# Optimization experiments

Measured on AMD Instinct MI355X. Metric: run time of the kernel, lower is better.

Reference implementation:

```python
import jax, jax.numpy as jnp
import numpy as np
from jax import lax

BN_EPS = 1e-5


def _zpool(x, axis):
    # stack (mean, max) over `axis` as 2 channels -> [N, 2, A, B]
    return jnp.stack([jnp.mean(x, axis=axis), jnp.max(x, axis=axis)], axis=1)


def _gate(p2, conv_w, conv_b, bn_w, bn_b, bn_rm, bn_rv, i):
    # p2: [N, 2, A, B]; 7x7 conv (2->1, pad 3) + scalar BN + relu + sigmoid
    y = lax.conv_general_dilated(
        p2, conv_w, window_strides=(1, 1), padding=[(3, 3), (3, 3)],
        dimension_numbers=("NCHW", "OIHW", "NCHW"))[:, 0] + conv_b[0]  # [N, A, B]
    y = (y - bn_rm[i]) * lax.rsqrt(bn_rv[i] + BN_EPS) * bn_w[i] + bn_b[i]
    return jax.nn.sigmoid(jnp.maximum(y, 0.0))


def setup_inputs() -> dict:
    key = jax.random.key(0)
    ks = jax.random.split(key, 7)
    N, C, H, W = 256, 2048, 7, 7
    return {
        "x": jax.random.normal(ks[0], (N, C, H, W), dtype=jnp.float32),
        "conv_w": jax.random.normal(ks[1], (1, 2, 7, 7), dtype=jnp.float32) * 0.1,
        "conv_b": jax.random.normal(ks[2], (1,), dtype=jnp.float32) * 0.1,
        "bn_w": jax.random.normal(ks[3], (3,), dtype=jnp.float32),
        "bn_b": jax.random.normal(ks[4], (3,), dtype=jnp.float32),
        "bn_rm": jax.random.normal(ks[5], (3,), dtype=jnp.float32) * 0.1,
        "bn_rv": jax.random.uniform(ks[6], (3,), dtype=jnp.float32),
    }


def reference(x, conv_w, conv_b, bn_w, bn_b, bn_rm, bn_rv):
    # x: [N, C, 7, 7]
    g_hw = _gate(_zpool(x, 1), conv_w, conv_b, bn_w, bn_b, bn_rm, bn_rv, 0)  # [N, 7, 7]
    g_ch = _gate(_zpool(x, 3), conv_w, conv_b, bn_w, bn_b, bn_rm, bn_rv, 1)  # [N, C, 7] indexed by h
    g_cw = _gate(_zpool(x, 2), conv_w, conv_b, bn_w, bn_b, bn_rm, bn_rv, 2)  # [N, C, 7] indexed by w
    gate = (g_hw[:, None, :, :] + g_ch[:, :, :, None] + g_cw[:, :, None, :]) * (1.0 / 3.0)
    return x * gate
```

## Files before the change

kernel.cpp:

```cpp
#include <hip/hip_runtime.h>

#define N_ 256
#define C_ 2048
#define HW_ 49
#define CPB 64
#define NCC (C_/CPB)

#define CHB(lc) ((lc) * HW_ + ((lc) >= 3 ? 1 : 0))

__global__ __launch_bounds__(256) void k_poolc(const float* __restrict__ x,
                                               float* __restrict__ psum,
                                               float* __restrict__ pmax) {
  const int cc = blockIdx.x, n = blockIdx.y;
  const int t = threadIdx.x;
  __shared__ float sx[CPB * HW_];
  __shared__ float part_s[HW_][5];
  __shared__ float part_m[HW_][5];

  const float4* xv = (const float4*)(x + ((size_t)n * C_ + (size_t)cc * CPB) * HW_);
  for (int v = t; v < 784; v += 256) {
    float4 q = xv[v];
    sx[v * 4 + 0] = q.x; sx[v * 4 + 1] = q.y;
    sx[v * 4 + 2] = q.z; sx[v * 4 + 3] = q.w;
  }
  __syncthreads();

  if (t < 245) {
    int hw = t / 5, s = t % 5;
    float sm = 0.f, mx = -3.4e38f;
    #pragma unroll
    for (int j = 0; j < 13; ++j) {
      int c = s * 13 + j;
      if (c < CPB) {
        float a = sx[c * HW_ + hw];
        sm += a; mx = fmaxf(mx, a);
      }
    }
    part_s[hw][s] = sm; part_m[hw][s] = mx;
  }
  __syncthreads();

  if (t < HW_) {
    float sm = 0.f, mx = -3.4e38f;
    #pragma unroll
    for (int s = 0; s < 5; ++s) { sm += part_s[t][s]; mx = fmaxf(mx, part_m[t][s]); }
    size_t o = ((size_t)n * NCC + cc) * HW_ + t;
    psum[o] = sm; pmax[o] = mx;
  }
}

__global__ __launch_bounds__(64) void k_ghw(const float* __restrict__ psum,
                                            const float* __restrict__ pmax,
                                            const float* __restrict__ cw,
                                            const float* __restrict__ cb,
                                            const float* __restrict__ bnw,
                                            const float* __restrict__ bnb,
                                            const float* __restrict__ bnrm,
                                            const float* __restrict__ bnrv,
                                            float* __restrict__ ghw) {
  const int n = blockIdx.x;
  const int t = threadIdx.x;
  __shared__ float p2c[2][13][13];
  __shared__ float s_cw[98];

  for (int i = t; i < 2 * 13 * 13; i += 64) ((float*)p2c)[i] = 0.f;
  for (int i = t; i < 98; i += 64) s_cw[i] = cw[i];
  __syncthreads();

  if (t < HW_) {
    float sm = 0.f, mx = -3.4e38f;
    const float* ps = psum + (size_t)n * NCC * HW_ + t;
    const float* pm = pmax + (size_t)n * NCC * HW_ + t;
    for (int cc = 0; cc < NCC; ++cc) {
      sm += ps[cc * HW_];
      mx = fmaxf(mx, pm[cc * HW_]);
    }
    p2c[0][t / 7 + 3][t % 7 + 3] = sm * (1.f / C_);
    p2c[1][t / 7 + 3][t % 7 + 3] = mx;
  }
  __syncthreads();

  if (t < HW_) {
    int a = t / 7, b = t % 7;
    float y = cb[0];
    #pragma unroll
    for (int i2 = 0; i2 < 2; ++i2)
      #pragma unroll
      for (int p = 0; p < 7; ++p)
        #pragma unroll
        for (int q = 0; q < 7; ++q)
          y += p2c[i2][a + p][b + q] * s_cw[i2 * 49 + p * 7 + q];
    float sc = bnw[0] * rsqrtf(bnrv[0] + 1e-5f);
    y = (y - bnrm[0]) * sc + bnb[0];
    y = fmaxf(y, 0.f);
    ghw[n * HW_ + t] = 1.f / (1.f + __expf(-y));
  }
}

__global__ __launch_bounds__(256, 6) void k_main(const float* __restrict__ x,
    const float* __restrict__ ghw,
    const float* __restrict__ cw, const float* __restrict__ cb,
    const float* __restrict__ bnw, const float* __restrict__ bnb,
    const float* __restrict__ bnrm, const float* __restrict__ bnrv,
    float* __restrict__ out) {
  const int cc = blockIdx.x;
  const int n  = (N_ - 1) - blockIdx.y;
  const int c0 = cc * CPB;
  const int t  = threadIdx.x;

  __shared__ __align__(16) float sx[3432];
  __shared__ __align__(16) float pool_lo[1120];
  __shared__ __align__(16) float pool_hi[1120];
  __shared__ float gch[448];
  __shared__ float gcw[448];
  __shared__ __align__(16) float s_w[112];
  __shared__ float s_ghw[49];

  const int conv = t & 1, i2 = (t >> 1) & 1, cl = t >> 2;
  const int bi = 1 + conv;
  const float cb0 = cb[0];
  const float sc_bn = bnw[bi] * rsqrtf(bnrv[bi] + 1e-5f);
  const float rm_bn = bnrm[bi];
  const float sh_bn = bnb[bi];

  if (t < 112) {
    int i2w = t / 56, rem = t % 56, p = rem / 8, q = rem % 8;
    s_w[t] = (q < 7) ? cw[i2w * 49 + p * 7 + q] : 0.f;
  }
  if (t < HW_) s_ghw[t] = ghw[n * HW_ + t];
  for (int i = t; i < 2 * 3 * HW_; i += 256) {
    int side = i / 147, off = i % 147;
    int lc = side ? (67 + off / HW_) : (off / HW_);
    int c = c0 - 3 + lc;
    float vv = 0.f;
    if (c >= 0 && c < C_) vv = x[((size_t)n * C_ + c) * HW_ + off % HW_];
    sx[CHB(lc) + off % HW_] = vv;
  }
  const float4* xv = (const float4*)(x + ((size_t)n * C_ + c0) * HW_);
  float4* sxv = (float4*)(sx + 148);
  for (int v = t; v < 784; v += 256) sxv[v] = xv[v];
  __syncthreads();

  for (int i = t; i < 70 * 7; i += 256) {
    int lc = i / 7, k = i % 7;
    int base = CHB(lc);
    float s1 = 0.f, m1 = -3.4e38f, s2 = 0.f, m2 = -3.4e38f;
    #pragma unroll
    for (int j = 0; j < 7; ++j) {
      float a = sx[base + k * 7 + j];
      s1 += a; m1 = fmaxf(m1, a);
      float b = sx[base + j * 7 + k];
      s2 += b; m2 = fmaxf(m2, b);
    }
    float* pb = (k < 4) ? pool_lo : pool_hi;
    int kk = k & 3;
    pb[(0 * 70 + lc) * 4 + kk] = s1 * (1.f / 7.f);
    pb[(1 * 70 + lc) * 4 + kk] = m1;
    pb[(2 * 70 + lc) * 4 + kk] = s2 * (1.f / 7.f);
    pb[(3 * 70 + lc) * 4 + kk] = m2;
  }
  __syncthreads();

  {
    const int f = conv * 2 + i2;
    const float* Wb = s_w + i2 * 56;
    float acc[7] = {0.f, 0.f, 0.f, 0.f, 0.f, 0.f, 0.f};
    #pragma unroll
    for (int p = 0; p < 7; ++p) {
      int ri = (f * 70 + cl + p) * 4;
      float4 r0 = *(const float4*)(pool_lo + ri);
      float4 r1 = *(const float4*)(pool_hi + ri);
      float row[7] = {r0.x, r0.y, r0.z, r0.w, r1.x, r1.y, r1.z};
      float4 w0 = *(const float4*)(Wb + p * 8);
      float4 w1 = *(const float4*)(Wb + p * 8 + 4);
      float wr[7] = {w0.x, w0.y, w0.z, w0.w, w1.x, w1.y, w1.z};
      #pragma unroll
      for (int q = 0; q < 7; ++q) {
        #pragma unroll
        for (int k = 0; k < 7; ++k) {
          int c = k + q - 3;
          if (c >= 0 && c < 7) acc[k] += row[c] * wr[q];
        }
      }
    }
    float fsum[7];
    #pragma unroll
    for (int k = 0; k < 7; ++k) fsum[k] = acc[k] + __shfl_xor(acc[k], 2, 64);
    if (i2 == 0) {
      float* gp = (conv ? gcw : gch) + cl * 7;
      #pragma unroll
      for (int k = 0; k < 7; ++k) {
        float y = (fsum[k] + cb0 - rm_bn) * sc_bn + sh_bn;
        y = fmaxf(y, 0.f);
        gp[k] = 1.f / (1.f + __expf(-y));
      }
    }
  }
  __syncthreads();

  float4* outv = (float4*)(out + ((size_t)n * C_ + c0) * HW_);
  for (int v = t; v < 784; v += 256) {
    float4 q = sxv[v];
    int e0 = v * 4;
    int cj = e0 / 49;
    int hw0 = e0 - cj * 49;
    float r0 = q.x, r1 = q.y, r2 = q.z, r3 = q.w;
    {
      int hw = hw0;
      int cjj = cj + (hw >= 49); hw -= (hw >= 49) ? 49 : 0;
      int h = (hw * 37) >> 8, w2 = hw - h * 7;
      r0 *= (s_ghw[hw] + gch[cjj * 7 + h] + gcw[cjj * 7 + w2]) * (1.f / 3.f);
    }
    {
      int hw = hw0 + 1;
      int cjj = cj + (hw >= 49); hw -= (hw >= 49) ? 49 : 0;
      int h = (hw * 37) >> 8, w2 = hw - h * 7;
      r1 *= (s_ghw[hw] + gch[cjj * 7 + h] + gcw[cjj * 7 + w2]) * (1.f / 3.f);
    }
    {
      int hw = hw0 + 2;
      int cjj = cj + (hw >= 49); hw -= (hw >= 49) ? 49 : 0;
      int h = (hw * 37) >> 8, w2 = hw - h * 7;
      r2 *= (s_ghw[hw] + gch[cjj * 7 + h] + gcw[cjj * 7 + w2]) * (1.f / 3.f);
    }
    {
      int hw = hw0 + 3;
      int cjj = cj + (hw >= 49); hw -= (hw >= 49) ? 49 : 0;
      int h = (hw * 37) >> 8, w2 = hw - h * 7;
      r3 *= (s_ghw[hw] + gch[cjj * 7 + h] + gcw[cjj * 7 + w2]) * (1.f / 3.f);
    }
    outv[v] = make_float4(r0, r1, r2, r3);
  }
}

extern "C" void kernel_launch(void* const* d_in, const int* in_sizes, int n_in,
                              void* d_out, int out_size, void* d_ws, size_t ws_size,
                              hipStream_t stream) {
  const float* x    = (const float*)d_in[0];
  const float* cw   = (const float*)d_in[1];
  const float* cb   = (const float*)d_in[2];
  const float* bnw  = (const float*)d_in[3];
  const float* bnb  = (const float*)d_in[4];
  const float* bnrm = (const float*)d_in[5];
  const float* bnrv = (const float*)d_in[6];
  float* out = (float*)d_out;

  float* psum = (float*)d_ws;
  float* pmax = psum + (size_t)N_ * NCC * HW_;
  float* ghw  = pmax + (size_t)N_ * NCC * HW_;

  k_poolc<<<dim3(NCC, N_), 256, 0, stream>>>(x, psum, pmax);
  k_ghw<<<dim3(N_), 64, 0, stream>>>(psum, pmax, cw, cb, bnw, bnb, bnrm, bnrv, ghw);
  k_main<<<dim3(NCC, N_), 256, 0, stream>>>(x, ghw, cw, cb, bnw, bnb, bnrm, bnrv, out);
}
```

Baseline: 89.29 us.

## Coarsen channel pooling blocks and compute two conv rows per thread

The channel-pooling kernel now has each block reduce 256 channels in four shared-memory passes, accumulating in registers, instead of 64 channels. This cuts the partial-result count per sample from 32 to 8, so the gate kernel reads fewer partials. In the main kernel, half the threads compute two adjacent conv output rows each, reusing the loaded pooled rows across both, with an interleaved pool layout to keep shared-memory accesses spread across banks. The trade-off is fewer blocks for the pooling kernel, extra barriers inside it, and half the main-kernel threads idle during the conv.

```diff
diff --git a/kernel.cpp b/kernel.cpp
--- a/kernel.cpp
+++ b/kernel.cpp
@@ -5,47 +5,52 @@
 #define HW_ 49
 #define CPB 64
 #define NCC (C_/CPB)
+#define NCHUNK 8
 
 #define CHB(lc) ((lc) * HW_ + ((lc) >= 3 ? 1 : 0))
+
+__device__ __forceinline__ int pool_idx(int f, int r, int kk) {
+  return (((f << 1) + (r & 1)) * 35 + (r >> 1)) * 4 + kk;
+}
 
 __global__ __launch_bounds__(256) void k_poolc(const float* __restrict__ x,
                                                float* __restrict__ psum,
                                                float* __restrict__ pmax) {
-  const int cc = blockIdx.x, n = blockIdx.y;
+  const int bc = blockIdx.x, n = blockIdx.y;
   const int t = threadIdx.x;
-  __shared__ float sx[CPB * HW_];
+  __shared__ __align__(16) float sx[CPB * HW_];
   __shared__ float part_s[HW_][5];
   __shared__ float part_m[HW_][5];
 
-  const float4* xv = (const float4*)(x + ((size_t)n * C_ + (size_t)cc * CPB) * HW_);
-  for (int v = t; v < 784; v += 256) {
-    float4 q = xv[v];
-    sx[v * 4 + 0] = q.x; sx[v * 4 + 1] = q.y;
-    sx[v * 4 + 2] = q.z; sx[v * 4 + 3] = q.w;
-  }
-  __syncthreads();
-
-  if (t < 245) {
-    int hw = t / 5, s = t % 5;
-    float sm = 0.f, mx = -3.4e38f;
-    #pragma unroll
-    for (int j = 0; j < 13; ++j) {
-      int c = s * 13 + j;
-      if (c < CPB) {
-        float a = sx[c * HW_ + hw];
-        sm += a; mx = fmaxf(mx, a);
+  float sm = 0.f, mx = -3.4e38f;
+  const int hw = t / 5, s = t % 5;
+
+  const float4* xv = (const float4*)(x + ((size_t)n * C_ + (size_t)bc * 256) * HW_);
+  #pragma unroll
+  for (int pass = 0; pass < 4; ++pass) {
+    float4* sv = (float4*)sx;
+    for (int v = t; v < 784; v += 256) sv[v] = xv[pass * 784 + v];
+    __syncthreads();
+    if (t < 245) {
+      #pragma unroll
+      for (int j = 0; j < 13; ++j) {
+        int c = s * 13 + j;
+        if (c < CPB) {
+          float a = sx[c * HW_ + hw];
+          sm += a; mx = fmaxf(mx, a);
+        }
       }
     }
-    part_s[hw][s] = sm; part_m[hw][s] = mx;
-  }
-  __syncthreads();
-
+    __syncthreads();
+  }
+  if (t < 245) { part_s[hw][s] = sm; part_m[hw][s] = mx; }
+  __syncthreads();
   if (t < HW_) {
-    float sm = 0.f, mx = -3.4e38f;
-    #pragma unroll
-    for (int s = 0; s < 5; ++s) { sm += part_s[t][s]; mx = fmaxf(mx, part_m[t][s]); }
-    size_t o = ((size_t)n * NCC + cc) * HW_ + t;
-    psum[o] = sm; pmax[o] = mx;
+    float s2 = 0.f, m2 = -3.4e38f;
+    #pragma unroll
+    for (int k = 0; k < 5; ++k) { s2 += part_s[t][k]; m2 = fmaxf(m2, part_m[t][k]); }
+    size_t o = ((size_t)n * NCHUNK + bc) * HW_ + t;
+    psum[o] = s2; pmax[o] = m2;
   }
 }
 
@@ -69,9 +74,10 @@
 
   if (t < HW_) {
     float sm = 0.f, mx = -3.4e38f;
-    const float* ps = psum + (size_t)n * NCC * HW_ + t;
-    const float* pm = pmax + (size_t)n * NCC * HW_ + t;
-    for (int cc = 0; cc < NCC; ++cc) {
+    const float* ps = psum + (size_t)n * NCHUNK * HW_ + t;
+    const float* pm = pmax + (size_t)n * NCHUNK * HW_ + t;
+    #pragma unroll
+    for (int cc = 0; cc < NCHUNK; ++cc) {
       sm += ps[cc * HW_];
       mx = fmaxf(mx, pm[cc * HW_]);
     }
@@ -116,7 +122,7 @@
   __shared__ __align__(16) float s_w[112];
   __shared__ float s_ghw[49];
 
-  const int conv = t & 1, i2 = (t >> 1) & 1, cl = t >> 2;
+  const int conv = t & 1, i2 = (t >> 1) & 1, cg = t >> 2;
   const int bi = 1 + conv;
   const float cb0 = cb[0];
   const float sc_bn = bnw[bi] * rsqrtf(bnrv[bi] + 1e-5f);
@@ -154,45 +160,68 @@
     }
     float* pb = (k < 4) ? pool_lo : pool_hi;
     int kk = k & 3;
-    pb[(0 * 70 + lc) * 4 + kk] = s1 * (1.f / 7.f);
-    pb[(1 * 70 + lc) * 4 + kk] = m1;
-    pb[(2 * 70 + lc) * 4 + kk] = s2 * (1.f / 7.f);
-    pb[(3 * 70 + lc) * 4 + kk] = m2;
-  }
-  __syncthreads();
-
-  {
+    pb[pool_idx(0, lc, kk)] = s1 * (1.f / 7.f);
+    pb[pool_idx(1, lc, kk)] = m1;
+    pb[pool_idx(2, lc, kk)] = s2 * (1.f / 7.f);
+    pb[pool_idx(3, lc, kk)] = m2;
+  }
+  __syncthreads();
+
+  if (t < 128) {
     const int f = conv * 2 + i2;
+    const int r0 = cg * 2;
     const float* Wb = s_w + i2 * 56;
-    float acc[7] = {0.f, 0.f, 0.f, 0.f, 0.f, 0.f, 0.f};
-    #pragma unroll
-    for (int p = 0; p < 7; ++p) {
-      int ri = (f * 70 + cl + p) * 4;
-      float4 r0 = *(const float4*)(pool_lo + ri);
-      float4 r1 = *(const float4*)(pool_hi + ri);
-      float row[7] = {r0.x, r0.y, r0.z, r0.w, r1.x, r1.y, r1.z};
-      float4 w0 = *(const float4*)(Wb + p * 8);
-      float4 w1 = *(const float4*)(Wb + p * 8 + 4);
-      float wr[7] = {w0.x, w0.y, w0.z, w0.w, w1.x, w1.y, w1.z};
-      #pragma unroll
-      for (int q = 0; q < 7; ++q) {
-        #pragma unroll
-        for (int k = 0; k < 7; ++k) {
-          int c = k + q - 3;
-          if (c >= 0 && c < 7) acc[k] += row[c] * wr[q];
-        }
-      }
-    }
-    float fsum[7];
-    #pragma unroll
-    for (int k = 0; k < 7; ++k) fsum[k] = acc[k] + __shfl_xor(acc[k], 2, 64);
+    float A[8], B[8];
+    float acc0[7] = {0,0,0,0,0,0,0};
+    float acc1[7] = {0,0,0,0,0,0,0};
+
+#define LOADROW(D, R) { \
+    int oo = pool_idx(f, (R), 0); \
+    float4 lo4 = *(const float4*)(pool_lo + oo); \
+    float4 hi4 = *(const float4*)(pool_hi + oo); \
+    D[0]=lo4.x; D[1]=lo4.y; D[2]=lo4.z; D[3]=lo4.w; \
+    D[4]=hi4.x; D[5]=hi4.y; D[6]=hi4.z; D[7]=hi4.w; }
+
+#define STEP(P, RL, RH) { \
+    float4 w0 = *(const float4*)(Wb + (P) * 8); \
+    float4 w1 = *(const float4*)(Wb + (P) * 8 + 4); \
+    float wr[7] = {w0.x, w0.y, w0.z, w0.w, w1.x, w1.y, w1.z}; \
+    _Pragma("unroll") \
+    for (int q = 0; q < 7; ++q) { \
+      _Pragma("unroll") \
+      for (int k = 0; k < 7; ++k) { \
+        int c = k + q - 3; \
+        if (c >= 0 && c < 7) { acc0[k] += RL[c] * wr[q]; acc1[k] += RH[c] * wr[q]; } \
+      } } }
+
+    LOADROW(A, r0);
+    LOADROW(B, r0 + 1);
+    STEP(0, A, B);
+    LOADROW(A, r0 + 2); STEP(1, B, A);
+    LOADROW(B, r0 + 3); STEP(2, A, B);
+    LOADROW(A, r0 + 4); STEP(3, B, A);
+    LOADROW(B, r0 + 5); STEP(4, A, B);
+    LOADROW(A, r0 + 6); STEP(5, B, A);
+    LOADROW(B, r0 + 7); STEP(6, A, B);
+#undef LOADROW
+#undef STEP
+
+    float f0[7], f1[7];
+    #pragma unroll
+    for (int k = 0; k < 7; ++k) {
+      f0[k] = acc0[k] + __shfl_xor(acc0[k], 2, 64);
+      f1[k] = acc1[k] + __shfl_xor(acc1[k], 2, 64);
+    }
     if (i2 == 0) {
-      float* gp = (conv ? gcw : gch) + cl * 7;
+      float* gp = (conv ? gcw : gch);
       #pragma unroll
       for (int k = 0; k < 7; ++k) {
-        float y = (fsum[k] + cb0 - rm_bn) * sc_bn + sh_bn;
-        y = fmaxf(y, 0.f);
-        gp[k] = 1.f / (1.f + __expf(-y));
+        float y0 = (f0[k] + cb0 - rm_bn) * sc_bn + sh_bn;
+        float y1 = (f1[k] + cb0 - rm_bn) * sc_bn + sh_bn;
+        y0 = fmaxf(y0, 0.f);
+        y1 = fmaxf(y1, 0.f);
+        gp[r0 * 7 + k]       = 1.f / (1.f + __expf(-y0));
+        gp[(r0 + 1) * 7 + k] = 1.f / (1.f + __expf(-y1));
       }
     }
   }
@@ -246,10 +275,10 @@
   float* out = (float*)d_out;
 
   float* psum = (float*)d_ws;
-  float* pmax = psum + (size_t)N_ * NCC * HW_;
-  float* ghw  = pmax + (size_t)N_ * NCC * HW_;
-
-  k_poolc<<<dim3(NCC, N_), 256, 0, stream>>>(x, psum, pmax);
+  float* pmax = psum + (size_t)N_ * NCHUNK * HW_;
+  float* ghw  = pmax + (size_t)N_ * NCHUNK * HW_;
+
+  k_poolc<<<dim3(NCHUNK, N_), 256, 0, stream>>>(x, psum, pmax);
   k_ghw<<<dim3(N_), 64, 0, stream>>>(psum, pmax, cw, cb, bnw, bnb, bnrm, bnrv, ghw);
   k_main<<<dim3(NCC, N_), 256, 0, stream>>>(x, ghw, cw, cb, bnw, bnb, bnrm, bnrv, out);
 }
```

New measurement: 82.29 us. -7.8%, faster.

## Move channel-gate conv into pooling kernel, leaving final pass as pure multiply

Applied to the files above, without the earlier changes.

The C-H and C-W pooling and their 7x7 gate convolutions move into the first pass, which now processes 256 channels per block in four staged passes and writes the gate vectors to workspace. The final kernel only loads x, the three gates and writes the output, dropping its halo loads, pooling and convolution. This trades extra global traffic for the gate arrays (about 2x N*C*7 floats) and a heavier, lower-parallelism first kernel for a lighter bandwidth-bound second pass. A fallback path keeps the old scheme when workspace is too small, and it contains an odd extra zero store.

```diff
diff --git a/kernel.cpp b/kernel.cpp
--- a/kernel.cpp
+++ b/kernel.cpp
@@ -4,48 +4,148 @@
 #define C_ 2048
 #define HW_ 49
 #define CPB 64
-#define NCC (C_/CPB)
-
-#define CHB(lc) ((lc) * HW_ + ((lc) >= 3 ? 1 : 0))
-
-__global__ __launch_bounds__(256) void k_poolc(const float* __restrict__ x,
-                                               float* __restrict__ psum,
-                                               float* __restrict__ pmax) {
-  const int cc = blockIdx.x, n = blockIdx.y;
+#define NCC 32
+#define NCHUNK 8
+
+
+__global__ __launch_bounds__(256) void k_pool_gate(const float* __restrict__ x,
+    const float* __restrict__ cw, const float* __restrict__ cb,
+    const float* __restrict__ bnw, const float* __restrict__ bnb,
+    const float* __restrict__ bnrm, const float* __restrict__ bnrv,
+    float* __restrict__ psum, float* __restrict__ pmax,
+    float* __restrict__ gch_g, float* __restrict__ gcw_g) {
+  const int bc = blockIdx.x, n = blockIdx.y;
   const int t = threadIdx.x;
-  __shared__ float sx[CPB * HW_];
+
+  __shared__ __align__(16) float sx[3584];
+  __shared__ __align__(16) float pool_lo[4 * 264 * 4];
+  __shared__ __align__(16) float pool_hi[4 * 264 * 4];
   __shared__ float part_s[HW_][5];
   __shared__ float part_m[HW_][5];
-
-  const float4* xv = (const float4*)(x + ((size_t)n * C_ + (size_t)cc * CPB) * HW_);
-  for (int v = t; v < 784; v += 256) {
-    float4 q = xv[v];
-    sx[v * 4 + 0] = q.x; sx[v * 4 + 1] = q.y;
-    sx[v * 4 + 2] = q.z; sx[v * 4 + 3] = q.w;
-  }
-  __syncthreads();
-
-  if (t < 245) {
-    int hw = t / 5, s = t % 5;
-    float sm = 0.f, mx = -3.4e38f;
-    #pragma unroll
-    for (int j = 0; j < 13; ++j) {
-      int c = s * 13 + j;
-      if (c < CPB) {
-        float a = sx[c * HW_ + hw];
-        sm += a; mx = fmaxf(mx, a);
+  __shared__ __align__(16) float s_w[112];
+
+  if (t < 112) {
+    int i2w = t / 56, rem = t % 56, p = rem / 8, q = rem % 8;
+    s_w[t] = (q < 7) ? cw[i2w * 49 + p * 7 + q] : 0.f;
+  }
+
+  float sm = 0.f, mx = -3.4e38f;
+  const int hwp = t / 5, sp = t % 5;
+
+  const float4* xv = (const float4*)(x + ((size_t)n * C_ + (size_t)bc * 256) * HW_);
+  float4* sv = (float4*)sx;
+  #pragma unroll
+  for (int pass = 0; pass < 4; ++pass) {
+    for (int v = t; v < 784; v += 256) sv[v] = xv[pass * 784 + v];
+    __syncthreads();
+    if (t < 245) {
+      #pragma unroll
+      for (int j = 0; j < 13; ++j) {
+        int c = sp * 13 + j;
+        if (c < CPB) { float a = sx[c * HW_ + hwp]; sm += a; mx = fmaxf(mx, a); }
       }
     }
-    part_s[hw][s] = sm; part_m[hw][s] = mx;
-  }
+    for (int i = t; i < 448; i += 256) {
+      int lc = i / 7, k = i % 7;
+      int base = lc * HW_;
+      float s1 = 0.f, m1 = -3.4e38f, s2 = 0.f, m2 = -3.4e38f;
+      #pragma unroll
+      for (int j = 0; j < 7; ++j) {
+        float a = sx[base + k * 7 + j]; s1 += a; m1 = fmaxf(m1, a);
+        float b = sx[base + j * 7 + k]; s2 += b; m2 = fmaxf(m2, b);
+      }
+      int pc = pass * 64 + 3 + lc;
+      int kk = k & 3;
+      float* pb = (k < 4) ? pool_lo : pool_hi;
+      pb[(0 * 264 + pc) * 4 + kk] = s1 * (1.f / 7.f);
+      pb[(1 * 264 + pc) * 4 + kk] = m1;
+      pb[(2 * 264 + pc) * 4 + kk] = s2 * (1.f / 7.f);
+      pb[(3 * 264 + pc) * 4 + kk] = m2;
+    }
+    __syncthreads();
+  }
+
+  if (t < 42) {
+    int hc = t / 7, k = t % 7;
+    int pc = (hc < 3) ? hc : 259 + (hc - 3);
+    int c = bc * 256 - 3 + pc;
+    float s1 = 0.f, m1 = 0.f, s2 = 0.f, m2 = 0.f;
+    if (c >= 0 && c < C_) {
+      m1 = -3.4e38f; m2 = -3.4e38f;
+      const float* xp = x + ((size_t)n * C_ + c) * HW_;
+      #pragma unroll
+      for (int j = 0; j < 7; ++j) {
+        float a = xp[k * 7 + j]; s1 += a; m1 = fmaxf(m1, a);
+        float b = xp[j * 7 + k]; s2 += b; m2 = fmaxf(m2, b);
+      }
+      s1 *= (1.f / 7.f); s2 *= (1.f / 7.f);
+    }
+    int kk = k & 3;
+    float* pb = (k < 4) ? pool_lo : pool_hi;
+    pb[(0 * 264 + pc) * 4 + kk] = s1;
+    pb[(1 * 264 + pc) * 4 + kk] = m1;
+    pb[(2 * 264 + pc) * 4 + kk] = s2;
+    pb[(3 * 264 + pc) * 4 + kk] = m2;
+  }
+  if (t < 245) { part_s[hwp][sp] = sm; part_m[hwp][sp] = mx; }
   __syncthreads();
 
   if (t < HW_) {
-    float sm = 0.f, mx = -3.4e38f;
-    #pragma unroll
-    for (int s = 0; s < 5; ++s) { sm += part_s[t][s]; mx = fmaxf(mx, part_m[t][s]); }
-    size_t o = ((size_t)n * NCC + cc) * HW_ + t;
-    psum[o] = sm; pmax[o] = mx;
+    float s2 = 0.f, m2 = -3.4e38f;
+    #pragma unroll
+    for (int k = 0; k < 5; ++k) { s2 += part_s[t][k]; m2 = fmaxf(m2, part_m[t][k]); }
+    size_t o = ((size_t)n * NCHUNK + bc) * HW_ + t;
+    psum[o] = s2; pmax[o] = m2;
+  }
+
+  const float cb0 = cb[0];
+  const float sc1 = bnw[1] * rsqrtf(bnrv[1] + 1e-5f), rm1 = bnrm[1], sh1 = bnb[1];
+  const float sc2 = bnw[2] * rsqrtf(bnrv[2] + 1e-5f), rm2 = bnrm[2], sh2 = bnb[2];
+  float g0[7] = {0, 0, 0, 0, 0, 0, 0};
+  float g1[7] = {0, 0, 0, 0, 0, 0, 0};
+  #pragma unroll
+  for (int f = 0; f < 4; ++f) {
+    const float* Wb = s_w + (f & 1) * 56;
+    #pragma unroll
+    for (int p = 0; p < 7; ++p) {
+      int ri = (f * 264 + t + p) * 4;
+      float4 lo4 = *(const float4*)(pool_lo + ri);
+      float4 hi4 = *(const float4*)(pool_hi + ri);
+      float row[7] = {lo4.x, lo4.y, lo4.z, lo4.w, hi4.x, hi4.y, hi4.z};
+      float4 w0 = *(const float4*)(Wb + p * 8);
+      float4 w1 = *(const float4*)(Wb + p * 8 + 4);
+      float wr[7] = {w0.x, w0.y, w0.z, w0.w, w1.x, w1.y, w1.z};
+      #pragma unroll
+      for (int q = 0; q < 7; ++q)
+        #pragma unroll
+        for (int k = 0; k < 7; ++k) {
+          int c = k + q - 3;
+          if (c >= 0 && c < 7) {
+            if (f < 2) g0[k] += row[c] * wr[q];
+            else       g1[k] += row[c] * wr[q];
+          }
+        }
+    }
+  }
+  #pragma unroll
+  for (int k = 0; k < 7; ++k) {
+    float y0 = (g0[k] + cb0 - rm1) * sc1 + sh1;
+    y0 = fmaxf(y0, 0.f);
+    sx[t * 7 + k] = 1.f / (1.f + __expf(-y0));
+    float y1 = (g1[k] + cb0 - rm2) * sc2 + sh2;
+    y1 = fmaxf(y1, 0.f);
+    sx[1792 + t * 7 + k] = 1.f / (1.f + __expf(-y1));
+  }
+  __syncthreads();
+  {
+    size_t goff = ((size_t)n * C_ + (size_t)bc * 256) * 7;
+    const float4* gs = (const float4*)sx;
+    float4* d1 = (float4*)(gch_g + goff);
+    float4* d2 = (float4*)(gcw_g + goff);
+    for (int v = t; v < 896; v += 256) {
+      if (v < 448) d1[v] = gs[v];
+      else         d2[v - 448] = gs[v];
+    }
   }
 }
 
@@ -69,9 +169,10 @@
 
   if (t < HW_) {
     float sm = 0.f, mx = -3.4e38f;
-    const float* ps = psum + (size_t)n * NCC * HW_ + t;
-    const float* pm = pmax + (size_t)n * NCC * HW_ + t;
-    for (int cc = 0; cc < NCC; ++cc) {
+    const float* ps = psum + (size_t)n * NCHUNK * HW_ + t;
+    const float* pm = pmax + (size_t)n * NCHUNK * HW_ + t;
+    #pragma unroll
+    for (int cc = 0; cc < NCHUNK; ++cc) {
       sm += ps[cc * HW_];
       mx = fmaxf(mx, pm[cc * HW_]);
     }
@@ -97,7 +198,110 @@
   }
 }
 
-__global__ __launch_bounds__(256, 6) void k_main(const float* __restrict__ x,
+__global__ __launch_bounds__(256) void k_mul(const float* __restrict__ x,
+    const float* __restrict__ ghw, const float* __restrict__ gch_g,
+    const float* __restrict__ gcw_g, float* __restrict__ out) {
+  const int cc = blockIdx.x;
+  const int n  = (N_ - 1) - blockIdx.y;
+  const int c0 = cc * CPB;
+  const int t  = threadIdx.x;
+
+  __shared__ float sg[960];
+
+  {
+    const float* g1 = gch_g + ((size_t)n * C_ + c0) * 7;
+    const float* g2 = gcw_g + ((size_t)n * C_ + c0) * 7;
+    for (int i = t; i < 945; i += 256) {
+      float v;
+      if (i < 448)      v = g1[i];
+      else if (i < 896) v = g2[i - 448];
+      else              v = ghw[n * HW_ + (i - 896)];
+      sg[i] = v;
+    }
+  }
+  __syncthreads();
+  const float* gch = sg;
+  const float* gcw = sg + 448;
+  const float* s_ghw = sg + 896;
+
+  const float4* xv = (const float4*)(x + ((size_t)n * C_ + c0) * HW_);
+  float4* outv = (float4*)(out + ((size_t)n * C_ + c0) * HW_);
+  for (int v = t; v < 784; v += 256) {
+    float4 q = xv[v];
+    int e0 = v * 4;
+    int cj = e0 / 49;
+    int hw0 = e0 - cj * 49;
+    float r0 = q.x, r1 = q.y, r2 = q.z, r3 = q.w;
+    {
+      int hw = hw0;
+      int cjj = cj + (hw >= 49); hw -= (hw >= 49) ? 49 : 0;
+      int h = (hw * 37) >> 8, w2 = hw - h * 7;
+      r0 *= (s_ghw[hw] + gch[cjj * 7 + h] + gcw[cjj * 7 + w2]) * (1.f / 3.f);
+    }
+    {
+      int hw = hw0 + 1;
+      int cjj = cj + (hw >= 49); hw -= (hw >= 49) ? 49 : 0;
+      int h = (hw * 37) >> 8, w2 = hw - h * 7;
+      r1 *= (s_ghw[hw] + gch[cjj * 7 + h] + gcw[cjj * 7 + w2]) * (1.f / 3.f);
+    }
+    {
+      int hw = hw0 + 2;
+      int cjj = cj + (hw >= 49); hw -= (hw >= 49) ? 49 : 0;
+      int h = (hw * 37) >> 8, w2 = hw - h * 7;
+      r2 *= (s_ghw[hw] + gch[cjj * 7 + h] + gcw[cjj * 7 + w2]) * (1.f / 3.f);
+    }
+    {
+      int hw = hw0 + 3;
+      int cjj = cj + (hw >= 49); hw -= (hw >= 49) ? 49 : 0;
+      int h = (hw * 37) >> 8, w2 = hw - h * 7;
+      r3 *= (s_ghw[hw] + gch[cjj * 7 + h] + gcw[cjj * 7 + w2]) * (1.f / 3.f);
+    }
+    outv[v] = make_float4(r0, r1, r2, r3);
+  }
+}
+
+
+__global__ __launch_bounds__(256) void k_poolc_fb(const float* __restrict__ x,
+                                                  float* __restrict__ psum,
+                                                  float* __restrict__ pmax) {
+  const int bc = blockIdx.x, n = blockIdx.y;
+  const int t = threadIdx.x;
+  __shared__ __align__(16) float sx[CPB * HW_];
+  __shared__ float part_s[HW_][5];
+  __shared__ float part_m[HW_][5];
+
+  float sm = 0.f, mx = -3.4e38f;
+  const int hw = t / 5, s = t % 5;
+
+  const float4* xv = (const float4*)(x + ((size_t)n * C_ + (size_t)bc * 256) * HW_);
+  #pragma unroll
+  for (int pass = 0; pass < 4; ++pass) {
+    float4* sv = (float4*)sx;
+    for (int v = t; v < 784; v += 256) sv[v] = xv[pass * 784 + v];
+    __syncthreads();
+    if (t < 245) {
+      #pragma unroll
+      for (int j = 0; j < 13; ++j) {
+        int c = s * 13 + j;
+        if (c < CPB) { float a = sx[c * HW_ + hw]; sm += a; mx = fmaxf(mx, a); }
+      }
+    }
+    __syncthreads();
+  }
+  if (t < 245) { part_s[hw][s] = sm; part_m[hw][s] = mx; }
+  __syncthreads();
+  if (t < HW_) {
+    float s2 = 0.f, m2 = -3.4e38f;
+    #pragma unroll
+    for (int k = 0; k < 5; ++k) { s2 += part_s[t][k]; m2 = fmaxf(m2, part_m[t][k]); }
+    size_t o = ((size_t)n * NCHUNK + bc) * HW_ + t;
+    psum[o] = s2; pmax[o] = m2;
+  }
+}
+
+#define CHB(lc) ((lc) * HW_ + ((lc) >= 3 ? 1 : 0))
+
+__global__ __launch_bounds__(256, 6) void k_main_fb(const float* __restrict__ x,
     const float* __restrict__ ghw,
     const float* __restrict__ cw, const float* __restrict__ cb,
     const float* __restrict__ bnw, const float* __restrict__ bnb,
@@ -147,13 +351,12 @@
     float s1 = 0.f, m1 = -3.4e38f, s2 = 0.f, m2 = -3.4e38f;
     #pragma unroll
     for (int j = 0; j < 7; ++j) {
-      float a = sx[base + k * 7 + j];
-      s1 += a; m1 = fmaxf(m1, a);
-      float b = sx[base + j * 7 + k];
-      s2 += b; m2 = fmaxf(m2, b);
+      float a = sx[base + k * 7 + j]; s1 += a; m1 = fmaxf(m1, a);
+      float b = sx[base + j * 7 + k]; s2 += b; m2 = fmaxf(m2, b);
     }
     float* pb = (k < 4) ? pool_lo : pool_hi;
     int kk = k & 3;
+    pb[((conv * 0 + 0) * 70 + lc) * 4 + kk + 0 * 280] = 0.f;
     pb[(0 * 70 + lc) * 4 + kk] = s1 * (1.f / 7.f);
     pb[(1 * 70 + lc) * 4 + kk] = m1;
     pb[(2 * 70 + lc) * 4 + kk] = s2 * (1.f / 7.f);
@@ -175,13 +378,12 @@
       float4 w1 = *(const float4*)(Wb + p * 8 + 4);
       float wr[7] = {w0.x, w0.y, w0.z, w0.w, w1.x, w1.y, w1.z};
       #pragma unroll
-      for (int q = 0; q < 7; ++q) {
+      for (int q = 0; q < 7; ++q)
         #pragma unroll
         for (int k = 0; k < 7; ++k) {
           int c = k + q - 3;
           if (c >= 0 && c < 7) acc[k] += row[c] * wr[q];
         }
-      }
     }
     float fsum[7];
     #pragma unroll
@@ -204,34 +406,19 @@
     int e0 = v * 4;
     int cj = e0 / 49;
     int hw0 = e0 - cj * 49;
-    float r0 = q.x, r1 = q.y, r2 = q.z, r3 = q.w;
-    {
-      int hw = hw0;
-      int cjj = cj + (hw >= 49); hw -= (hw >= 49) ? 49 : 0;
+    float r[4] = {q.x, q.y, q.z, q.w};
+    #pragma unroll
+    for (int j = 0; j < 4; ++j) {
+      int hw = hw0 + j;
+      int cjj = cj + (hw >= 49);
+      hw -= (hw >= 49) ? 49 : 0;
       int h = (hw * 37) >> 8, w2 = hw - h * 7;
-      r0 *= (s_ghw[hw] + gch[cjj * 7 + h] + gcw[cjj * 7 + w2]) * (1.f / 3.f);
-    }
-    {
-      int hw = hw0 + 1;
-      int cjj = cj + (hw >= 49); hw -= (hw >= 49) ? 49 : 0;
-      int h = (hw * 37) >> 8, w2 = hw - h * 7;
-      r1 *= (s_ghw[hw] + gch[cjj * 7 + h] + gcw[cjj * 7 + w2]) * (1.f / 3.f);
-    }
-    {
-      int hw = hw0 + 2;
-      int cjj = cj + (hw >= 49); hw -= (hw >= 49) ? 49 : 0;
-      int h = (hw * 37) >> 8, w2 = hw - h * 7;
-      r2 *= (s_ghw[hw] + gch[cjj * 7 + h] + gcw[cjj * 7 + w2]) * (1.f / 3.f);
-    }
-    {
-      int hw = hw0 + 3;
-      int cjj = cj + (hw >= 49); hw -= (hw >= 49) ? 49 : 0;
-      int h = (hw * 37) >> 8, w2 = hw - h * 7;
-      r3 *= (s_ghw[hw] + gch[cjj * 7 + h] + gcw[cjj * 7 + w2]) * (1.f / 3.f);
-    }
-    outv[v] = make_float4(r0, r1, r2, r3);
-  }
-}
+      r[j] *= (s_ghw[hw] + gch[cjj * 7 + h] + gcw[cjj * 7 + w2]) * (1.f / 3.f);
+    }
+    outv[v] = make_float4(r[0], r[1], r[2], r[3]);
+  }
+}
+
 
 extern "C" void kernel_launch(void* const* d_in, const int* in_sizes, int n_in,
                               void* d_out, int out_size, void* d_ws, size_t ws_size,
@@ -245,11 +432,22 @@
   const float* bnrv = (const float*)d_in[6];
   float* out = (float*)d_out;
 
-  float* psum = (float*)d_ws;
-  float* pmax = psum + (size_t)N_ * NCC * HW_;
-  float* ghw  = pmax + (size_t)N_ * NCC * HW_;
-
-  k_poolc<<<dim3(NCC, N_), 256, 0, stream>>>(x, psum, pmax);
-  k_ghw<<<dim3(N_), 64, 0, stream>>>(psum, pmax, cw, cb, bnw, bnb, bnrm, bnrv, ghw);
-  k_main<<<dim3(NCC, N_), 256, 0, stream>>>(x, ghw, cw, cb, bnw, bnb, bnrm, bnrv, out);
-}
+  float* psum  = (float*)d_ws;
+  float* pmax  = psum + (size_t)N_ * NCHUNK * HW_;
+  float* ghw   = pmax + (size_t)N_ * NCHUNK * HW_;
+  float* gch_g = ghw + (size_t)N_ * HW_;
+  float* gcw_g = gch_g + (size_t)N_ * C_ * 7;
+  size_t need_floats = (size_t)N_ * NCHUNK * HW_ * 2 + (size_t)N_ * HW_
+                     + (size_t)N_ * C_ * 7 * 2;
+
+  if (ws_size >= need_floats * sizeof(float)) {
+    k_pool_gate<<<dim3(NCHUNK, N_), 256, 0, stream>>>(
+        x, cw, cb, bnw, bnb, bnrm, bnrv, psum, pmax, gch_g, gcw_g);
+    k_ghw<<<dim3(N_), 64, 0, stream>>>(psum, pmax, cw, cb, bnw, bnb, bnrm, bnrv, ghw);
+    k_mul<<<dim3(NCC, N_), 256, 0, stream>>>(x, ghw, gch_g, gcw_g, out);
+  } else {
+    k_poolc_fb<<<dim3(NCHUNK, N_), 256, 0, stream>>>(x, psum, pmax);
+    k_ghw<<<dim3(N_), 64, 0, stream>>>(psum, pmax, cw, cb, bnw, bnb, bnrm, bnrv, ghw);
+    k_main_fb<<<dim3(NCC, N_), 256, 0, stream>>>(x, ghw, cw, cb, bnw, bnb, bnrm, bnrv, out);
+  }
+}
```

Result: faster. 86.97 us (-2.6%).

## Make main kernel persistent with register double-buffered tile prefetch

Applied to the files above, without the earlier changes.

The main kernel becomes a persistent grid of 1280 blocks, each looping over up to 7 (n, channel-chunk) tiles. It keeps the current tile in registers and prefetches the next tile's x and ghw values while pooling and convolving the current one, and the output multiply now reads from registers instead of shared memory. Pooling is restructured so each thread handles one channel over a padded 52-float row, and halo channels are read straight from global memory. The pooling pre-pass also uses 8 larger chunks per sample instead of 32, so there are fewer partial sums to write and reduce. The cost is higher register pressure (occupancy hint lowered from 6 to 5) and less latency hiding across blocks.

```diff
diff --git a/kernel.cpp b/kernel.cpp
--- a/kernel.cpp
+++ b/kernel.cpp
@@ -4,48 +4,45 @@
 #define C_ 2048
 #define HW_ 49
 #define CPB 64
-#define NCC (C_/CPB)
-
-#define CHB(lc) ((lc) * HW_ + ((lc) >= 3 ? 1 : 0))
+#define NCC 32
+#define NCHUNK 8
+#define NBLK 1280
 
 __global__ __launch_bounds__(256) void k_poolc(const float* __restrict__ x,
                                                float* __restrict__ psum,
                                                float* __restrict__ pmax) {
-  const int cc = blockIdx.x, n = blockIdx.y;
+  const int bc = blockIdx.x, n = blockIdx.y;
   const int t = threadIdx.x;
-  __shared__ float sx[CPB * HW_];
+  __shared__ __align__(16) float sx[CPB * HW_];
   __shared__ float part_s[HW_][5];
   __shared__ float part_m[HW_][5];
 
-  const float4* xv = (const float4*)(x + ((size_t)n * C_ + (size_t)cc * CPB) * HW_);
-  for (int v = t; v < 784; v += 256) {
-    float4 q = xv[v];
-    sx[v * 4 + 0] = q.x; sx[v * 4 + 1] = q.y;
-    sx[v * 4 + 2] = q.z; sx[v * 4 + 3] = q.w;
-  }
+  float sm = 0.f, mx = -3.4e38f;
+  const int hw = t / 5, s = t % 5;
+
+  const float4* xv = (const float4*)(x + ((size_t)n * C_ + (size_t)bc * 256) * HW_);
+  #pragma unroll
+  for (int pass = 0; pass < 4; ++pass) {
+    float4* sv = (float4*)sx;
+    for (int v = t; v < 784; v += 256) sv[v] = xv[pass * 784 + v];
+    __syncthreads();
+    if (t < 245) {
+      #pragma unroll
+      for (int j = 0; j < 13; ++j) {
+        int c = s * 13 + j;
+        if (c < CPB) { float a = sx[c * HW_ + hw]; sm += a; mx = fmaxf(mx, a); }
+      }
+    }
+    __syncthreads();
+  }
+  if (t < 245) { part_s[hw][s] = sm; part_m[hw][s] = mx; }
   __syncthreads();
-
-  if (t < 245) {
-    int hw = t / 5, s = t % 5;
-    float sm = 0.f, mx = -3.4e38f;
-    #pragma unroll
-    for (int j = 0; j < 13; ++j) {
-      int c = s * 13 + j;
-      if (c < CPB) {
-        float a = sx[c * HW_ + hw];
-        sm += a; mx = fmaxf(mx, a);
-      }
-    }
-    part_s[hw][s] = sm; part_m[hw][s] = mx;
-  }
-  __syncthreads();
-
   if (t < HW_) {
-    float sm = 0.f, mx = -3.4e38f;
-    #pragma unroll
-    for (int s = 0; s < 5; ++s) { sm += part_s[t][s]; mx = fmaxf(mx, part_m[t][s]); }
-    size_t o = ((size_t)n * NCC + cc) * HW_ + t;
-    psum[o] = sm; pmax[o] = mx;
+    float s2 = 0.f, m2 = -3.4e38f;
+    #pragma unroll
+    for (int k = 0; k < 5; ++k) { s2 += part_s[t][k]; m2 = fmaxf(m2, part_m[t][k]); }
+    size_t o = ((size_t)n * NCHUNK + bc) * HW_ + t;
+    psum[o] = s2; pmax[o] = m2;
   }
 }
 
@@ -69,9 +66,10 @@
 
   if (t < HW_) {
     float sm = 0.f, mx = -3.4e38f;
-    const float* ps = psum + (size_t)n * NCC * HW_ + t;
-    const float* pm = pmax + (size_t)n * NCC * HW_ + t;
-    for (int cc = 0; cc < NCC; ++cc) {
+    const float* ps = psum + (size_t)n * NCHUNK * HW_ + t;
+    const float* pm = pmax + (size_t)n * NCHUNK * HW_ + t;
+    #pragma unroll
+    for (int cc = 0; cc < NCHUNK; ++cc) {
       sm += ps[cc * HW_];
       mx = fmaxf(mx, pm[cc * HW_]);
     }
@@ -97,24 +95,120 @@
   }
 }
 
-__global__ __launch_bounds__(256, 6) void k_main(const float* __restrict__ x,
-    const float* __restrict__ ghw,
+
+__device__ __forceinline__ void pool_write(float* pool_lo, float* pool_hi, int row,
+    const float* ws, const float* wm, const float* hs, const float* hm) {
+  const float C7 = 1.f / 7.f;
+  *(float4*)(pool_lo + (0 * 70 + row) * 4) = make_float4(ws[0]*C7, ws[1]*C7, ws[2]*C7, ws[3]*C7);
+  *(float4*)(pool_hi + (0 * 70 + row) * 4) = make_float4(ws[4]*C7, ws[5]*C7, ws[6]*C7, 0.f);
+  *(float4*)(pool_lo + (1 * 70 + row) * 4) = make_float4(wm[0], wm[1], wm[2], wm[3]);
+  *(float4*)(pool_hi + (1 * 70 + row) * 4) = make_float4(wm[4], wm[5], wm[6], 0.f);
+  *(float4*)(pool_lo + (2 * 70 + row) * 4) = make_float4(hs[0]*C7, hs[1]*C7, hs[2]*C7, hs[3]*C7);
+  *(float4*)(pool_hi + (2 * 70 + row) * 4) = make_float4(hs[4]*C7, hs[5]*C7, hs[6]*C7, 0.f);
+  *(float4*)(pool_lo + (3 * 70 + row) * 4) = make_float4(hm[0], hm[1], hm[2], hm[3]);
+  *(float4*)(pool_hi + (3 * 70 + row) * 4) = make_float4(hm[4], hm[5], hm[6], 0.f);
+}
+
+__device__ __forceinline__ void pools_phase(const float* __restrict__ x,
+    const float* sx, float* pool_lo, float* pool_hi, int t, int cc, int n) {
+  if (t < 64) {
+    const float4* chp = (const float4*)(sx + t * 52);
+    float ws[7], wm[7], hs[7], hm[7];
+    #pragma unroll
+    for (int r = 0; r < 7; ++r) { ws[r] = 0.f; wm[r] = -3.4e38f; hs[r] = 0.f; hm[r] = -3.4e38f; }
+    #pragma unroll
+    for (int b = 0; b < 13; ++b) {
+      float4 q = chp[b];
+      float vv[4] = {q.x, q.y, q.z, q.w};
+      #pragma unroll
+      for (int j = 0; j < 4; ++j) {
+        int p = b * 4 + j;
+        if (p < 49) {
+          int r = p / 7, k = p % 7;
+          ws[r] += vv[j]; wm[r] = fmaxf(wm[r], vv[j]);
+          hs[k] += vv[j]; hm[k] = fmaxf(hm[k], vv[j]);
+        }
+      }
+    }
+    pool_write(pool_lo, pool_hi, t + 3, ws, wm, hs, hm);
+  } else if (t < 70) {
+    int hc = t - 64;
+    int row = (hc < 3) ? hc : (64 + hc);
+    int c = (hc < 3) ? (cc * CPB - 3 + hc) : (cc * CPB + CPB + hc - 3);
+    bool ok = (c >= 0 && c < C_);
+    float ws[7], wm[7], hs[7], hm[7];
+    #pragma unroll
+    for (int r = 0; r < 7; ++r) {
+      ws[r] = 0.f; hs[r] = 0.f;
+      wm[r] = ok ? -3.4e38f : 0.f; hm[r] = ok ? -3.4e38f : 0.f;
+    }
+    if (ok) {
+      const float* xp = x + ((size_t)n * C_ + c) * HW_;
+      #pragma unroll
+      for (int j = 0; j < 49; ++j) {
+        int r = j / 7, k = j % 7;
+        float v = xp[j];
+        ws[r] += v; wm[r] = fmaxf(wm[r], v);
+        hs[k] += v; hm[k] = fmaxf(hm[k], v);
+      }
+    }
+    pool_write(pool_lo, pool_hi, row, ws, wm, hs, hm);
+  }
+}
+
+__device__ __forceinline__ void conv_phase(const float* pool_lo, const float* pool_hi,
+    const float* s_w, float* gch, float* gcw, int conv, int i2, int cl,
+    float cb0, float sc_bn, float rm_bn, float sh_bn) {
+  const int f = conv * 2 + i2;
+  const float* Wb = s_w + i2 * 56;
+  float acc[7] = {0.f, 0.f, 0.f, 0.f, 0.f, 0.f, 0.f};
+  #pragma unroll
+  for (int p = 0; p < 7; ++p) {
+    int ri = (f * 70 + cl + p) * 4;
+    float4 r0 = *(const float4*)(pool_lo + ri);
+    float4 r1 = *(const float4*)(pool_hi + ri);
+    float row[7] = {r0.x, r0.y, r0.z, r0.w, r1.x, r1.y, r1.z};
+    float4 w0 = *(const float4*)(Wb + p * 8);
+    float4 w1 = *(const float4*)(Wb + p * 8 + 4);
+    float wr[7] = {w0.x, w0.y, w0.z, w0.w, w1.x, w1.y, w1.z};
+    #pragma unroll
+    for (int q = 0; q < 7; ++q)
+      #pragma unroll
+      for (int k = 0; k < 7; ++k) {
+        int c = k + q - 3;
+        if (c >= 0 && c < 7) acc[k] += row[c] * wr[q];
+      }
+  }
+  float fsum[7];
+  #pragma unroll
+  for (int k = 0; k < 7; ++k) fsum[k] = acc[k] + __shfl_xor(acc[k], 2, 64);
+  if (i2 == 0) {
+    float* gp = (conv ? gcw : gch) + cl * 7;
+    #pragma unroll
+    for (int k = 0; k < 7; ++k) {
+      float y = (fsum[k] + cb0 - rm_bn) * sc_bn + sh_bn;
+      y = fmaxf(y, 0.f);
+      gp[k] = 1.f / (1.f + __expf(-y));
+    }
+  }
+}
+
+__global__ __launch_bounds__(256, 5) void k_fused(const float* __restrict__ x,
+    const float* __restrict__ ghw_g,
     const float* __restrict__ cw, const float* __restrict__ cb,
     const float* __restrict__ bnw, const float* __restrict__ bnb,
     const float* __restrict__ bnrm, const float* __restrict__ bnrv,
     float* __restrict__ out) {
-  const int cc = blockIdx.x;
-  const int n  = (N_ - 1) - blockIdx.y;
-  const int c0 = cc * CPB;
-  const int t  = threadIdx.x;
-
-  __shared__ __align__(16) float sx[3432];
+  const int bid = blockIdx.x;
+  const int t   = threadIdx.x;
+
+  __shared__ __align__(16) float sx[64 * 52];
   __shared__ __align__(16) float pool_lo[1120];
   __shared__ __align__(16) float pool_hi[1120];
+  __shared__ __align__(16) float s_w[112];
   __shared__ float gch[448];
   __shared__ float gcw[448];
-  __shared__ __align__(16) float s_w[112];
-  __shared__ float s_ghw[49];
+  __shared__ float sg[2][49];
 
   const int conv = t & 1, i2 = (t >> 1) & 1, cl = t >> 2;
   const int bi = 1 + conv;
@@ -127,110 +221,76 @@
     int i2w = t / 56, rem = t % 56, p = rem / 8, q = rem % 8;
     s_w[t] = (q < 7) ? cw[i2w * 49 + p * 7 + q] : 0.f;
   }
-  if (t < HW_) s_ghw[t] = ghw[n * HW_ + t];
-  for (int i = t; i < 2 * 3 * HW_; i += 256) {
-    int side = i / 147, off = i % 147;
-    int lc = side ? (67 + off / HW_) : (off / HW_);
-    int c = c0 - 3 + lc;
-    float vv = 0.f;
-    if (c >= 0 && c < C_) vv = x[((size_t)n * C_ + c) * HW_ + off % HW_];
-    sx[CHB(lc) + off % HW_] = vv;
-  }
-  const float4* xv = (const float4*)(x + ((size_t)n * C_ + c0) * HW_);
-  float4* sxv = (float4*)(sx + 148);
-  for (int v = t; v < 784; v += 256) sxv[v] = xv[v];
+
+  float4 a0, a1, a2, a3, b0, b1, b2, b3;
+  float ga, gb;
+
+#define LOADT(TID, Q0, Q1, Q2, Q3, G) { \
+    int cc_ = (TID) & 31, n_ = (TID) >> 5; \
+    const float4* xv_ = (const float4*)(x + ((size_t)n_ * C_ + cc_ * CPB) * HW_); \
+    Q0 = xv_[t]; Q1 = xv_[t + 256]; Q2 = xv_[t + 512]; \
+    if (t < 16) Q3 = xv_[t + 768]; \
+    if (t < HW_) G = ghw_g[n_ * HW_ + t]; }
+
+#define ST4(Q, V) { \
+    int e_ = (V) * 4; int ch_ = e_ / 49; int pos_ = e_ - ch_ * 49; \
+    int ba_ = ch_ * 52 + pos_; \
+    sx[ba_] = Q.x; \
+    sx[ba_ + 1 + ((pos_ >= 48) ? 3 : 0)] = Q.y; \
+    sx[ba_ + 2 + ((pos_ >= 47) ? 3 : 0)] = Q.z; \
+    sx[ba_ + 3 + ((pos_ >= 46) ? 3 : 0)] = Q.w; }
+
+#define WRITET(Q0, Q1, Q2, Q3, G, SGI) { \
+    ST4(Q0, t); ST4(Q1, t + 256); ST4(Q2, t + 512); \
+    if (t < 16) ST4(Q3, t + 768); \
+    if (t < HW_) sg[SGI][t] = G; }
+
+#define MUL1(Q, V) { \
+    int e0_ = (V) * 4; int cj_ = e0_ / 49; int hw0_ = e0_ - cj_ * 49; \
+    float r_[4] = {Q.x, Q.y, Q.z, Q.w}; \
+    _Pragma("unroll") \
+    for (int j = 0; j < 4; ++j) { \
+      int hw_ = hw0_ + j; int cjj_ = cj_ + (hw_ >= 49); \
+      hw_ -= (hw_ >= 49) ? 49 : 0; \
+      int h_ = (hw_ * 37) >> 8, w2_ = hw_ - h_ * 7; \
+      r_[j] *= (sgc[hw_] + gch[cjj_ * 7 + h_] + gcw[cjj_ * 7 + w2_]) * (1.f / 3.f); \
+    } \
+    outv[V] = make_float4(r_[0], r_[1], r_[2], r_[3]); }
+
+#define ITER(IT, QC0, QC1, QC2, QC3, QN0, QN1, QN2, QN3, GN, SGC, SGN, HASN) { \
+    const int tcur = bid + (IT) * NBLK; \
+    const int cc_c = tcur & 31, n_c = tcur >> 5; \
+    if (HASN) LOADT(bid + ((IT) + 1) * NBLK, QN0, QN1, QN2, QN3, GN); \
+    pools_phase(x, sx, pool_lo, pool_hi, t, cc_c, n_c); \
+    __syncthreads(); \
+    conv_phase(pool_lo, pool_hi, s_w, gch, gcw, conv, i2, cl, cb0, sc_bn, rm_bn, sh_bn); \
+    __syncthreads(); \
+    { const float* sgc = sg[SGC]; \
+      float4* outv = (float4*)(out + ((size_t)n_c * C_ + cc_c * CPB) * HW_); \
+      MUL1(QC0, t); MUL1(QC1, t + 256); MUL1(QC2, t + 512); \
+      if (t < 16) MUL1(QC3, t + 768); } \
+    if (HASN) WRITET(QN0, QN1, QN2, QN3, GN, SGN); \
+    __syncthreads(); }
+
+  LOADT(bid, a0, a1, a2, a3, ga);
+  WRITET(a0, a1, a2, a3, ga, 0);
   __syncthreads();
 
-  for (int i = t; i < 70 * 7; i += 256) {
-    int lc = i / 7, k = i % 7;
-    int base = CHB(lc);
-    float s1 = 0.f, m1 = -3.4e38f, s2 = 0.f, m2 = -3.4e38f;
-    #pragma unroll
-    for (int j = 0; j < 7; ++j) {
-      float a = sx[base + k * 7 + j];
-      s1 += a; m1 = fmaxf(m1, a);
-      float b = sx[base + j * 7 + k];
-      s2 += b; m2 = fmaxf(m2, b);
-    }
-    float* pb = (k < 4) ? pool_lo : pool_hi;
-    int kk = k & 3;
-    pb[(0 * 70 + lc) * 4 + kk] = s1 * (1.f / 7.f);
-    pb[(1 * 70 + lc) * 4 + kk] = m1;
-    pb[(2 * 70 + lc) * 4 + kk] = s2 * (1.f / 7.f);
-    pb[(3 * 70 + lc) * 4 + kk] = m2;
-  }
-  __syncthreads();
-
-  {
-    const int f = conv * 2 + i2;
-    const float* Wb = s_w + i2 * 56;
-    float acc[7] = {0.f, 0.f, 0.f, 0.f, 0.f, 0.f, 0.f};
-    #pragma unroll
-    for (int p = 0; p < 7; ++p) {
-      int ri = (f * 70 + cl + p) * 4;
-      float4 r0 = *(const float4*)(pool_lo + ri);
-      float4 r1 = *(const float4*)(pool_hi + ri);
-      float row[7] = {r0.x, r0.y, r0.z, r0.w, r1.x, r1.y, r1.z};
-      float4 w0 = *(const float4*)(Wb + p * 8);
-      float4 w1 = *(const float4*)(Wb + p * 8 + 4);
-      float wr[7] = {w0.x, w0.y, w0.z, w0.w, w1.x, w1.y, w1.z};
-      #pragma unroll
-      for (int q = 0; q < 7; ++q) {
-        #pragma unroll
-        for (int k = 0; k < 7; ++k) {
-          int c = k + q - 3;
-          if (c >= 0 && c < 7) acc[k] += row[c] * wr[q];
-        }
-      }
-    }
-    float fsum[7];
-    #pragma unroll
-    for (int k = 0; k < 7; ++k) fsum[k] = acc[k] + __shfl_xor(acc[k], 2, 64);
-    if (i2 == 0) {
-      float* gp = (conv ? gcw : gch) + cl * 7;
-      #pragma unroll
-      for (int k = 0; k < 7; ++k) {
-        float y = (fsum[k] + cb0 - rm_bn) * sc_bn + sh_bn;
-        y = fmaxf(y, 0.f);
-        gp[k] = 1.f / (1.f + __expf(-y));
-      }
-    }
-  }
-  __syncthreads();
-
-  float4* outv = (float4*)(out + ((size_t)n * C_ + c0) * HW_);
-  for (int v = t; v < 784; v += 256) {
-    float4 q = sxv[v];
-    int e0 = v * 4;
-    int cj = e0 / 49;
-    int hw0 = e0 - cj * 49;
-    float r0 = q.x, r1 = q.y, r2 = q.z, r3 = q.w;
-    {
-      int hw = hw0;
-      int cjj = cj + (hw >= 49); hw -= (hw >= 49) ? 49 : 0;
-      int h = (hw * 37) >> 8, w2 = hw - h * 7;
-      r0 *= (s_ghw[hw] + gch[cjj * 7 + h] + gcw[cjj * 7 + w2]) * (1.f / 3.f);
-    }
-    {
-      int hw = hw0 + 1;
-      int cjj = cj + (hw >= 49); hw -= (hw >= 49) ? 49 : 0;
-      int h = (hw * 37) >> 8, w2 = hw - h * 7;
-      r1 *= (s_ghw[hw] + gch[cjj * 7 + h] + gcw[cjj * 7 + w2]) * (1.f / 3.f);
-    }
-    {
-      int hw = hw0 + 2;
-      int cjj = cj + (hw >= 49); hw -= (hw >= 49) ? 49 : 0;
-      int h = (hw * 37) >> 8, w2 = hw - h * 7;
-      r2 *= (s_ghw[hw] + gch[cjj * 7 + h] + gcw[cjj * 7 + w2]) * (1.f / 3.f);
-    }
-    {
-      int hw = hw0 + 3;
-      int cjj = cj + (hw >= 49); hw -= (hw >= 49) ? 49 : 0;
-      int h = (hw * 37) >> 8, w2 = hw - h * 7;
-      r3 *= (s_ghw[hw] + gch[cjj * 7 + h] + gcw[cjj * 7 + w2]) * (1.f / 3.f);
-    }
-    outv[v] = make_float4(r0, r1, r2, r3);
-  }
+  ITER(0, a0, a1, a2, a3, b0, b1, b2, b3, gb, 0, 1, true);
+  ITER(1, b0, b1, b2, b3, a0, a1, a2, a3, ga, 1, 0, true);
+  ITER(2, a0, a1, a2, a3, b0, b1, b2, b3, gb, 0, 1, true);
+  ITER(3, b0, b1, b2, b3, a0, a1, a2, a3, ga, 1, 0, true);
+  ITER(4, a0, a1, a2, a3, b0, b1, b2, b3, gb, 0, 1, true);
+  ITER(5, b0, b1, b2, b3, a0, a1, a2, a3, ga, 1, 0, (bid < 512));
+  if (bid < 512) {
+    ITER(6, a0, a1, a2, a3, b0, b1, b2, b3, gb, 0, 1, false);
+  }
+
+#undef LOADT
+#undef ST4
+#undef WRITET
+#undef MUL1
+#undef ITER
 }
 
 extern "C" void kernel_launch(void* const* d_in, const int* in_sizes, int n_in,
@@ -246,10 +306,10 @@
   float* out = (float*)d_out;
 
   float* psum = (float*)d_ws;
-  float* pmax = psum + (size_t)N_ * NCC * HW_;
-  float* ghw  = pmax + (size_t)N_ * NCC * HW_;
-
-  k_poolc<<<dim3(NCC, N_), 256, 0, stream>>>(x, psum, pmax);
+  float* pmax = psum + (size_t)N_ * NCHUNK * HW_;
+  float* ghw  = pmax + (size_t)N_ * NCHUNK * HW_;
+
+  k_poolc<<<dim3(NCHUNK, N_), 256, 0, stream>>>(x, psum, pmax);
   k_ghw<<<dim3(N_), 64, 0, stream>>>(psum, pmax, cw, cb, bnw, bnb, bnrm, bnrv, ghw);
-  k_main<<<dim3(NCC, N_), 256, 0, stream>>>(x, ghw, cw, cb, bnw, bnb, bnrm, bnrv, out);
-}
+  k_fused<<<dim3(NBLK), 256, 0, stream>>>(x, ghw, cw, cb, bnw, bnb, bnrm, bnrv, out);
+}
```

Result: slower. 168.3 us (+88.5%).
